# Optimization experiments

Hardware: AMD Instinct MI355X
Metric: run time of the kernel (lower is better)

Reference implementation:

```python
import jax, jax.numpy as jnp
import numpy as np

LN_EPS = 1e-5

def _mha(xq, xkv, in_w, in_b, out_w, out_b, n_heads):
    # torch nn.MultiheadAttention, batch_first=True, dropout=0
    B, S, d = xq.shape
    T = xkv.shape[1]
    dh = d // n_heads
    wq, wk, wv = jnp.split(in_w, 3, axis=0)   # each [d, d]
    bq, bk, bv = jnp.split(in_b, 3)
    q = (xq @ wq.T + bq).reshape(B, S, n_heads, dh).transpose(0, 2, 1, 3)
    k = (xkv @ wk.T + bk).reshape(B, T, n_heads, dh).transpose(0, 2, 1, 3)
    v = (xkv @ wv.T + bv).reshape(B, T, n_heads, dh).transpose(0, 2, 1, 3)
    scores = jnp.einsum('bhsd,bhtd->bhst', q, k) / jnp.sqrt(jnp.asarray(dh, xq.dtype))
    attn = jax.nn.softmax(scores, axis=-1)    # explicit [B,H,S,T] weights (need_weights=True path)
    o = jnp.einsum('bhst,bhtd->bhsd', attn, v)
    o = o.transpose(0, 2, 1, 3).reshape(B, S, d)
    return o @ out_w.T + out_b

def _ln(x, g, b):
    mu = jnp.mean(x, axis=-1, keepdims=True)
    var = jnp.mean(jnp.square(x - mu), axis=-1, keepdims=True)
    return (x - mu) / jnp.sqrt(var + LN_EPS) * g + b

def setup_inputs() -> dict:
    key = jax.random.key(0)
    B, S, T, d, ff = 4, 1024, 1024, 1024, 4096
    ks = jax.random.split(key, 10)
    s = 0.02
    return {
        'x': jax.random.normal(ks[0], (B, S, d), jnp.float32),
        'mem': jax.random.normal(ks[1], (B, T, d), jnp.float32),
        'sa_in_w': jax.random.normal(ks[2], (3 * d, d), jnp.float32) * s,
        'sa_in_b': jnp.zeros((3 * d,), jnp.float32),
        'sa_out_w': jax.random.normal(ks[3], (d, d), jnp.float32) * s,
        'sa_out_b': jnp.zeros((d,), jnp.float32),
        'ca_in_w': jax.random.normal(ks[4], (3 * d, d), jnp.float32) * s,
        'ca_in_b': jnp.zeros((3 * d,), jnp.float32),
        'ca_out_w': jax.random.normal(ks[5], (d, d), jnp.float32) * s,
        'ca_out_b': jnp.zeros((d,), jnp.float32),
        'ff_w1': jax.random.normal(ks[6], (ff, d), jnp.float32) * s,
        'ff_b1': jnp.zeros((ff,), jnp.float32),
        'ff_w2': jax.random.normal(ks[7], (d, ff), jnp.float32) * s,
        'ff_b2': jnp.zeros((d,), jnp.float32),
        'ln1_g': jnp.ones((d,), jnp.float32), 'ln1_b': jnp.zeros((d,), jnp.float32),
        'ln2_g': jnp.ones((d,), jnp.float32), 'ln2_b': jnp.zeros((d,), jnp.float32),
        'ln3_g': jnp.ones((d,), jnp.float32), 'ln3_b': jnp.zeros((d,), jnp.float32),
        'n_heads': 16,
    }

def reference(x, mem, sa_in_w, sa_in_b, sa_out_w, sa_out_b,
              ca_in_w, ca_in_b, ca_out_w, ca_out_b,
              ff_w1, ff_b1, ff_w2, ff_b2,
              ln1_g, ln1_b, ln2_g, ln2_b, ln3_g, ln3_b, n_heads):
    sa = _mha(x, x, sa_in_w, sa_in_b, sa_out_w, sa_out_b, n_heads)
    x = _ln(x + sa, ln1_g, ln1_b)
    ca = _mha(x, mem, ca_in_w, ca_in_b, ca_out_w, ca_out_b, n_heads)
    x = _ln(x + ca, ln2_g, ln2_b)
    h = jax.nn.gelu(x @ ff_w1.T + ff_b1, approximate=False)  # torch nn.GELU default = exact erf
    ff = h @ ff_w2.T + ff_b2
    return _ln(x + ff, ln3_g, ln3_b)
```

## Files before the change

### kernel.cpp

```cpp
#include <hip/hip_runtime.h>
#include <cstddef>

#define D_MODEL 1024
#define SEQ     1024
#define BATCH   4
#define NHEAD   16
#define DH      64
#define FFDIM   4096
#define NTOK    (BATCH*SEQ)

typedef float f32x4  __attribute__((ext_vector_type(4)));
typedef short bf16x8 __attribute__((ext_vector_type(8)));

static __device__ __forceinline__ unsigned short f2bf(float x){
  union { float f; unsigned u; } v; v.f = x;
  unsigned r = v.u + 0x7fffu + ((v.u >> 16) & 1u);
  return (unsigned short)(r >> 16);
}

static __device__ __forceinline__ unsigned short f2bf_t(float x){
  union { float f; unsigned u; } v; v.f = x;
  return (unsigned short)(v.u >> 16);
}

static __device__ __forceinline__ float bf2f(unsigned short h){
  union { unsigned u; float f; } v; v.u = ((unsigned)h) << 16; return v.f;
}

static __device__ __forceinline__ float fast_exp2(float x){
#if __has_builtin(__builtin_amdgcn_exp2f)
  return __builtin_amdgcn_exp2f(x);
#else
  return __expf(x * 0.69314718056f);
#endif
}

static __device__ __forceinline__ void gl_lds16(const void* g, void* l){
  __builtin_amdgcn_global_load_lds((const __attribute__((address_space(1))) void*)g,
                                   (__attribute__((address_space(3))) void*)l, 16, 0, 0);
}

#define WAITV(n) asm volatile("s_waitcnt vmcnt(" #n ")" ::: "memory")
#define WAITL0() asm volatile("s_waitcnt lgkmcnt(0)" ::: "memory")
#define SBAR()   __builtin_amdgcn_s_barrier()
#define SCHED0() __builtin_amdgcn_sched_barrier(0)

static __device__ __forceinline__ int2 swz_tile(int gx, int RX, int RY){
  int id = blockIdx.y * gx + blockIdx.x;
  int x = id & 7, s = id >> 3;
  int nrx = gx / RX;
  int bx = (x % nrx) * RX + (s % RX);
  int by = (x / nrx) * RY + (s / RX);
  return make_int2(bx, by);
}

struct CvtJobs {
  const float* src[8];
  unsigned short* dst[8];
  int n[8];
};

__global__ __launch_bounds__(256) void cvt_kernel(CvtJobs jobs){
  int seg = blockIdx.y;
  const float* s = jobs.src[seg];
  unsigned short* d = jobs.dst[seg];
  int n = jobs.n[seg];
  int stride = gridDim.x * 256 * 4;
  for (int i = (blockIdx.x*256 + threadIdx.x)*4; i < n; i += stride){
    float4 v = *(const float4*)(s + i);
    ushort4 o;
    o.x = f2bf(v.x); o.y = f2bf(v.y); o.z = f2bf(v.z); o.w = f2bf(v.w);
    *(ushort4*)(d + i) = o;
  }
}

static __device__ __forceinline__ int cidx(int row, int col){
  return row*128 + (((col >> 3) ^ (row & 15)) << 3) + (col & 7);
}

template<int EPI>
static __device__ __forceinline__ void gemm_core(
    unsigned short* smem,
    const unsigned short* __restrict__ A,
    const unsigned short* __restrict__ B,
    const float* __restrict__ bias,
    void* __restrict__ out0,
    unsigned short* __restrict__ vt,
    int N, int K, int kbeg, int kend, int row0, int col0,
    int split, int ldout)
{
  unsigned short* As = smem;
  unsigned short* Bs = smem + 128*64;
  const int tid  = threadIdx.x;
  const int w    = tid >> 6, lane = tid & 63;
  const int quad = lane >> 4, l15 = lane & 15;
  const int lr   = lane >> 3, lc = lane & 7;
  const int csrc = lc ^ lr;
  const int sw   = l15 & 7;
  const int wm = (w >> 1) * 64, wn = (w & 1) * 64;

  f32x4 acc[4][4];
  const f32x4 zero4 = {0.f, 0.f, 0.f, 0.f};
  #pragma unroll
  for (int i=0;i<4;i++)
    #pragma unroll
    for (int j=0;j<4;j++)
      acc[i][j] = zero4;

  const unsigned short* Ag = A + (size_t)(row0 + lr)*K + csrc*8;
  const unsigned short* Bg = B + (size_t)(col0 + lr)*K + csrc*8;

  for (int k0 = kbeg; k0 < kend; k0 += 64){
    #pragma unroll
    for (int i=0;i<4;i++){
      gl_lds16(Ag + (size_t)(i*32 + w*8)*K + k0, &As[i*2048 + w*512]);
      gl_lds16(Bg + (size_t)(i*32 + w*8)*K + k0, &Bs[i*2048 + w*512]);
    }
    __syncthreads();
    #pragma unroll
    for (int ks=0; ks<2; ks++){
      bf16x8 af[4], bfr[4];
      #pragma unroll
      for (int i=0;i<4;i++)
        af[i] = *(const bf16x8*)&As[(wm + i*16 + l15)*64 + ((ks*4 + quad) ^ sw)*8];
      #pragma unroll
      for (int j=0;j<4;j++)
        bfr[j] = *(const bf16x8*)&Bs[(wn + j*16 + l15)*64 + ((ks*4 + quad) ^ sw)*8];
      #pragma unroll
      for (int i=0;i<4;i++)
        #pragma unroll
        for (int j=0;j<4;j++)
          acc[i][j] = __builtin_amdgcn_mfma_f32_16x16x32_bf16(af[i], bfr[j], acc[i][j], 0, 0, 0);
    }
    __syncthreads();
  }

  float bj[4];
  #pragma unroll
  for (int j=0;j<4;j++) bj[j] = bias[col0 + wn + j*16 + l15];

  unsigned short* Cs = smem;

  #pragma unroll
  for (int i=0;i<4;i++){
    #pragma unroll
    for (int r=0;r<4;r++){
      int lrow = wm + i*16 + quad*4 + r;
      #pragma unroll
      for (int j=0;j<4;j++){
        int lcol = wn + j*16 + l15;
        float v = acc[i][j][r] + bj[j];
        Cs[cidx(lrow, lcol)] = f2bf(v);
      }
    }
  }
  __syncthreads();

  const int ld = N;
  #pragma unroll
  for (int p=0;p<2;p++){
    int c = p*64 + (tid >> 2);
    unsigned short* dst = (unsigned short*)out0 + (size_t)(row0 + c)*ld + col0;
    #pragma unroll
    for (int k=0;k<4;k++){
      int m = (tid & 3) + k*4;
      bf16x8 val = *(const bf16x8*)&Cs[c*128 + ((m ^ (c & 15)) << 3)];
      *(bf16x8*)(dst + m*8) = val;
    }
  }
}

__global__ __launch_bounds__(256) void gemm_split(
    const unsigned short* A, const unsigned short* B, const float* bias,
    unsigned short* outA, unsigned short* outB, int N, int K)
{
  __shared__ __align__(16) unsigned short smem[2*128*64];
  int2 t = swz_tile(gridDim.x, 4, 8);
  int kseg = K >> 1;
  int kbeg = blockIdx.z * kseg;
  unsigned short* o = blockIdx.z ? outB : outA;
  gemm_core<1>(smem, A, B, bias, o, nullptr, N, K, kbeg, kbeg + kseg,
               t.y*128, t.x*128, 0, 0);
}

#define G256_LDB(bufp) do{                                                    \
    const unsigned short* Bs_ = (bufp) + 16384;                               \
    _Pragma("unroll")                                                         \
    for (int ks=0; ks<2; ks++){                                               \
      const int ch = ((ks*4 + quad) ^ sw)*8;                                  \
      _Pragma("unroll")                                                       \
      for (int j=0;j<4;j++)                                                   \
        bfr[ks][j] = *(const bf16x8*)&Bs_[(wc*64 + j*16 + l15)*64 + ch];      \
    }                                                                         \
  }while(0)

#define G256_LDA(bufp, S) do{                                                 \
    const unsigned short* As_ = (bufp);                                       \
    _Pragma("unroll")                                                         \
    for (int ks=0; ks<2; ks++){                                               \
      const int ch = ((ks*4 + quad) ^ sw)*8;                                  \
      afr[ks][0] = *(const bf16x8*)&As_[(wr*128 + (2*(S)  )*16 + l15)*64 + ch]; \
      afr[ks][1] = *(const bf16x8*)&As_[(wr*128 + (2*(S)+1)*16 + l15)*64 + ch]; \
    }                                                                         \
  }while(0)

#define G256_PH(S) do{                                                        \
    __builtin_amdgcn_s_setprio(1);                                            \
    _Pragma("unroll")                                                         \
    for (int ks=0; ks<2; ks++){                                               \
      _Pragma("unroll")                                                       \
      for (int j=0;j<4;j++){                                                  \
        acc[2*(S)  ][j] = __builtin_amdgcn_mfma_f32_16x16x32_bf16(afr[ks][0], bfr[ks][j], acc[2*(S)  ][j], 0, 0, 0); \
        acc[2*(S)+1][j] = __builtin_amdgcn_mfma_f32_16x16x32_bf16(afr[ks][1], bfr[ks][j], acc[2*(S)+1][j], 0, 0, 0); \
      }                                                                       \
    }                                                                         \
    __builtin_amdgcn_s_setprio(0);                                            \
  }while(0)

#define STG_B4(k0, dstp) do{ unsigned short* _d=(dstp); const int _k=(k0);    \
    gl_lds16(Bg + (size_t)(0*64 + w*8)*K + _k, _d + 16384 + 0*4096 + w*512);  \
    gl_lds16(Bg + (size_t)(1*64 + w*8)*K + _k, _d + 16384 + 1*4096 + w*512);  \
    gl_lds16(Bg + (size_t)(2*64 + w*8)*K + _k, _d + 16384 + 2*4096 + w*512);  \
    gl_lds16(Bg + (size_t)(3*64 + w*8)*K + _k, _d + 16384 + 3*4096 + w*512);  \
  }while(0)
#define STG_A02(k0, dstp) do{ unsigned short* _d=(dstp); const int _k=(k0);   \
    gl_lds16(Ag + (size_t)(0*64 + w*8)*K + _k, _d + 0*4096 + w*512);          \
    gl_lds16(Ag + (size_t)(2*64 + w*8)*K + _k, _d + 2*4096 + w*512);          \
  }while(0)
#define STG_A13(k0, dstp) do{ unsigned short* _d=(dstp); const int _k=(k0);   \
    gl_lds16(Ag + (size_t)(1*64 + w*8)*K + _k, _d + 1*4096 + w*512);          \
    gl_lds16(Ag + (size_t)(3*64 + w*8)*K + _k, _d + 3*4096 + w*512);          \
  }while(0)

template<int EPI>
static __device__ __forceinline__ void gemm256_core(
    unsigned short* smem,
    const unsigned short* __restrict__ A,
    const unsigned short* __restrict__ B,
    const float* __restrict__ bias,
    void* __restrict__ out0,
    unsigned short* __restrict__ vt,
    int N, int K, int kbeg, int kend, int row0, int col0,
    int split, int ldout)
{
  const int tid  = threadIdx.x;
  const int w    = tid >> 6, lane = tid & 63;
  const int quad = lane >> 4, l15 = lane & 15;
  const int lr   = lane >> 3, lc = lane & 7;
  const int csrc = lc ^ lr;
  const int sw   = l15 & 7;
  const int wr   = w >> 2, wc = w & 3;

  f32x4 acc[8][4];
  const f32x4 zero4 = {0.f, 0.f, 0.f, 0.f};
  #pragma unroll
  for (int i=0;i<8;i++)
    #pragma unroll
    for (int j=0;j<4;j++)
      acc[i][j] = zero4;

  bf16x8 bfr[2][4];
  bf16x8 afr[2][2];

  const unsigned short* Ag = A + (size_t)(row0 + lr)*K + csrc*8;
  const unsigned short* Bg = B + (size_t)(col0 + lr)*K + csrc*8;

  unsigned short* buf0 = smem;
  unsigned short* buf1 = smem + 32768;

  STG_B4(kbeg, buf0); STG_A02(kbeg, buf0); STG_A13(kbeg, buf0);
  STG_B4(kbeg + 64, buf1); STG_A02(kbeg + 64, buf1);

  for (int t = 0; t < 16; t++){
    unsigned short* cur = (t & 1) ? buf1 : buf0;
    unsigned short* oth = (t & 1) ? buf0 : buf1;
    const int kb = kbeg + t*64;
    if (t < 15) { WAITV(6); } else { WAITV(0); }
    SBAR(); SCHED0();
    G256_LDB(cur); G256_LDA(cur, 0);
    if (t < 15) STG_A13(kb + 64, oth);
    G256_PH(0);
    WAITL0(); SBAR(); SCHED0();
    G256_LDA(cur, 1);
    if (t < 14) STG_B4(kb + 128, cur);
    G256_PH(1);
    WAITL0(); SBAR(); SCHED0();
    G256_LDA(cur, 2);
    if (t < 14) STG_A02(kb + 128, cur);
    G256_PH(2);
    WAITL0(); SBAR(); SCHED0();
    G256_LDA(cur, 3);
    G256_PH(3);
    WAITL0();
  }
  SBAR(); SCHED0();

  float bj[4];
  #pragma unroll
  for (int j=0;j<4;j++) bj[j] = bias[col0 + wc*64 + j*16 + l15];

  const bool vtile = (EPI == 5) && (col0 >= split);
  unsigned short* Cs = smem;

  #pragma unroll
  for (int i=0;i<8;i++){
    #pragma unroll
    for (int r=0;r<4;r++){
      int lrow = wr*128 + i*16 + quad*4 + r;
      #pragma unroll
      for (int j=0;j<4;j++){
        int lcol = wc*64 + j*16 + l15;
        float v = acc[i][j][r] + bj[j];
        if (EPI == 2){
          float t = 0.7978845608f * (v + 0.044715f * v * v * v);
          float e = __expf(2.f * t);
          float th = 1.f - 2.f * __builtin_amdgcn_rcpf(e + 1.f);
          v = 0.5f * v * (1.f + th);
        }
        int rr = vtile ? lcol : lrow, cc = vtile ? lrow : lcol;
        Cs[rr*256 + (((cc >> 3) ^ (rr & 31)) << 3) + (cc & 7)] = f2bf(v);
      }
    }
  }
  __syncthreads();

  const int ld = (EPI == 5) ? ldout : N;
  #pragma unroll
  for (int p=0;p<2;p++){
    int c = p*128 + (tid >> 2);
    unsigned short* dst;
    if (!vtile){
      dst = (unsigned short*)out0 + (size_t)(row0 + c)*ld + col0;
    } else {
      int colg = (col0 - split) + c;
      int hh = colg >> 6, dd = colg & 63;
      int bb = row0 >> 10, t0 = row0 & 1023;
      dst = vt + ((size_t)(bb*NHEAD + hh)*DH + dd)*SEQ + t0;
    }
    #pragma unroll
    for (int k=0;k<8;k++){
      int m = (tid & 3) + k*4;
      bf16x8 val = *(const bf16x8*)&Cs[c*256 + ((m ^ (c & 31)) << 3)];
      *(bf16x8*)(dst + m*8) = val;
    }
  }
}

__global__ __launch_bounds__(512, 2) void gemm256_ffn1(
    const unsigned short* A, const unsigned short* B, const float* bias,
    unsigned short* out0, int N, int K)
{
  __shared__ __align__(16) unsigned short smem[2*2*256*64];
  int2 t = swz_tile(gridDim.x, 4, 8);
  gemm256_core<2>(smem, A, B, bias, out0, nullptr, N, K, 0, K,
                  t.y*256, t.x*256, 0, 0);
}

__global__ __launch_bounds__(512, 2) void gemm_kv256(
    const unsigned short* xb, const unsigned short* memb,
    const unsigned short* wsa, const unsigned short* wca,
    const float* bsa, const float* bca,
    unsigned short* ksa, unsigned short* vtsa,
    unsigned short* kca, unsigned short* vtca)
{
  __shared__ __align__(16) unsigned short smem[2*2*256*64];
  const int id = blockIdx.x;
  const int xcd = id & 7, s = id >> 3;
  const bool sa = s < 16;
  const int u = sa ? s : s - 16;
  const int bx = (xcd & 3)*2 + (u & 1);
  const int by = (xcd >> 2)*8 + (u >> 1);
  gemm256_core<5>(smem, sa ? xb : memb, sa ? wsa : wca, sa ? bsa : bca,
                  sa ? ksa : kca, sa ? vtsa : vtca,
                  2048, 1024, 0, 1024, by*256, bx*256, 1024, 1024);
}

__global__ __launch_bounds__(512, 2) void gemm256_split4(
    const unsigned short* A, const unsigned short* B, const float* bias,
    unsigned short* o0, unsigned short* o1, unsigned short* o2, unsigned short* o3,
    int N, int K)
{
  __shared__ __align__(16) unsigned short smem[2*2*256*64];
  const int id = blockIdx.x;
  const int xcd = id & 7, s = id >> 3;
  const int z  = xcd >> 1;
  const int bx = s & 3;
  const int by = (xcd & 1)*8 + (s >> 2);
  const int kseg = K >> 2, kbeg = z * kseg;
  unsigned short* o = (z == 0) ? o0 : (z == 1) ? o1 : (z == 2) ? o2 : o3;
  gemm256_core<1>(smem, A, B, bias, o, nullptr, N, K, kbeg, kbeg + kseg,
                  by*256, bx*256, 0, 0);
}

__global__ __launch_bounds__(256) void attn_kernel(
    const unsigned short* __restrict__ Xa,
    const unsigned short* __restrict__ Wq,
    const float* __restrict__ bq,
    const unsigned short* __restrict__ Kp,
    const unsigned short* __restrict__ Vt,
    unsigned short* __restrict__ O)
{
  __shared__ __align__(16) unsigned short Ks[64*64];
  __shared__ __align__(16) unsigned short Vs[64*64];
  __shared__ __align__(16) unsigned short Bu[4*16*72];

  const int tid  = threadIdx.x;
  const int w    = tid >> 6, lane = tid & 63;
  const int quad = lane >> 4, l15 = lane & 15;
  const int lr   = lane >> 3, lc = lane & 7;
  const int csrc = lc ^ lr;
  const int sw   = l15 & 7;
  const int id = blockIdx.x;
  const int xc = id & 7, s = id >> 3;
  const int bh = xc*8 + (s >> 4), qt = s & 15;
  const int b = bh >> 4, h = bh & 15;
  const int q0   = qt * 64;
  const int tok0 = b * SEQ;
  const int hoff = h * DH;

  const f32x4 zero4 = {0.f, 0.f, 0.f, 0.f};

  f32x4 qacc[4];
  #pragma unroll
  for (int dj=0;dj<4;dj++) qacc[dj] = zero4;

  const unsigned short* Ag = Xa + (size_t)(tok0 + q0 + lr)*1024 + csrc*8;
  const unsigned short* Wg = Wq + (size_t)(hoff + lr)*1024 + csrc*8;

  for (int k0 = 0; k0 < 1024; k0 += 64){
    #pragma unroll
    for (int i=0;i<2;i++)
      gl_lds16(Ag + (size_t)(i*32 + w*8)*1024 + k0, &Bu[i*2048 + w*512]);
    #pragma unroll
    for (int i=0;i<2;i++)
      gl_lds16(Wg + (size_t)(i*32 + w*8)*1024 + k0, &Ks[i*2048 + w*512]);
    __syncthreads();
    #pragma unroll
    for (int ks=0; ks<2; ks++){
      const int ch = ((ks*4 + quad) ^ sw)*8;
      bf16x8 af = *(const bf16x8*)&Bu[(w*16 + l15)*64 + ch];
      bf16x8 bfr[4];
      #pragma unroll
      for (int dj=0;dj<4;dj++)
        bfr[dj] = *(const bf16x8*)&Ks[(dj*16 + l15)*64 + ch];
      #pragma unroll
      for (int dj=0;dj<4;dj++)
        qacc[dj] = __builtin_amdgcn_mfma_f32_16x16x32_bf16(af, bfr[dj], qacc[dj], 0, 0, 0);
    }
    __syncthreads();
  }

  {
    const float QSCALE = 0.125f * 1.44269504f;
    float biasv[4];
    #pragma unroll
    for (int dj=0;dj<4;dj++) biasv[dj] = bq[hoff + dj*16 + l15];
    #pragma unroll
    for (int dj=0;dj<4;dj++)
      #pragma unroll
      for (int r=0;r<4;r++){
        int q = w*16 + quad*4 + r;
        int d = dj*16 + l15;
        Bu[q*64 + (((d>>3) ^ (q&7))<<3) + (d&7)] = f2bf((qacc[dj][r] + biasv[dj]) * QSCALE);
      }
  }
  __syncthreads();

  bf16x8 qb[2];
  {
    int row = w*16 + l15;
    qb[0] = *(const bf16x8*)&Bu[row*64 + ((0 + quad) ^ sw)*8];
    qb[1] = *(const bf16x8*)&Bu[row*64 + ((4 + quad) ^ sw)*8];
  }

  float lsum = 0.f;
  f32x4 oacc[4];
  #pragma unroll
  for (int dt=0;dt<4;dt++) oacc[dt] = zero4;

  unsigned short* pw = &Bu[w*16*72];

  for (int kc = 0; kc < SEQ/64; ++kc){
    __syncthreads();
    #pragma unroll
    for (int i=0;i<2;i++){
      int r = i*32 + w*8 + lr;
      gl_lds16(Kp + (size_t)(tok0 + kc*64 + r)*1024 + hoff + csrc*8, &Ks[i*2048 + w*512]);
      gl_lds16(Vt + ((size_t)bh*DH + r)*SEQ + kc*64 + csrc*8,        &Vs[i*2048 + w*512]);
    }
    __syncthreads();

    #pragma unroll
    for (int tj=0;tj<4;tj++){
      bf16x8 ka0 = *(const bf16x8*)&Ks[(tj*16 + l15)*64 + ((0 + quad) ^ sw)*8];
      bf16x8 ka1 = *(const bf16x8*)&Ks[(tj*16 + l15)*64 + ((4 + quad) ^ sw)*8];
      f32x4 z = zero4;
      __builtin_amdgcn_s_setprio(1);
      z = __builtin_amdgcn_mfma_f32_16x16x32_bf16(ka0, qb[0], z, 0, 0, 0);
      z = __builtin_amdgcn_mfma_f32_16x16x32_bf16(ka1, qb[1], z, 0, 0, 0);
      __builtin_amdgcn_s_setprio(0);
      float p0 = fast_exp2(z[0]);
      float p1 = fast_exp2(z[1]);
      float p2 = fast_exp2(z[2]);
      float p3 = fast_exp2(z[3]);
      lsum += (p0 + p1) + (p2 + p3);
      short4 pk;
      pk.x = (short)f2bf_t(p0); pk.y = (short)f2bf_t(p1);
      pk.z = (short)f2bf_t(p2); pk.w = (short)f2bf_t(p3);
      *(short4*)&pw[l15*72 + tj*16 + quad*4] = pk;
    }

    __builtin_amdgcn_s_setprio(1);
    {
      bf16x8 pa0 = *(const bf16x8*)&pw[l15*72 + quad*8];
      bf16x8 pa1 = *(const bf16x8*)&pw[l15*72 + 32 + quad*8];
      #pragma unroll
      for (int dt=0;dt<4;dt++){
        bf16x8 vb0 = *(const bf16x8*)&Vs[(dt*16 + l15)*64 + ((0 + quad) ^ sw)*8];
        bf16x8 vb1 = *(const bf16x8*)&Vs[(dt*16 + l15)*64 + ((4 + quad) ^ sw)*8];
        oacc[dt] = __builtin_amdgcn_mfma_f32_16x16x32_bf16(pa0, vb0, oacc[dt], 0, 0, 0);
        oacc[dt] = __builtin_amdgcn_mfma_f32_16x16x32_bf16(pa1, vb1, oacc[dt], 0, 0, 0);
      }
    }
    __builtin_amdgcn_s_setprio(0);
  }

  lsum += __shfl_xor(lsum, 16);
  lsum += __shfl_xor(lsum, 32);

  __syncthreads();
  unsigned short* OB = Bu;
  #pragma unroll
  for (int r=0;r<4;r++){
    float lv = __shfl(lsum, quad*4 + r);
    float rinv = __builtin_amdgcn_rcpf(lv);
    int q = w*16 + quad*4 + r;
    #pragma unroll
    for (int dt=0;dt<4;dt++){
      int d = dt*16 + l15;
      OB[q*64 + (((d>>3) ^ (q&7))<<3) + (d&7)] = f2bf(oacc[dt][r] * rinv);
    }
  }
  __syncthreads();
  {
    int q = tid >> 2;
    unsigned short* dst = O + (size_t)(tok0 + q0 + q)*D_MODEL + hoff;
    #pragma unroll
    for (int k=0;k<2;k++){
      int m = (tid & 3) + k*4;
      bf16x8 val = *(const bf16x8*)&OB[q*64 + ((m ^ (q & 7)) << 3)];
      *(bf16x8*)(dst + m*8) = val;
    }
  }
}

__global__ __launch_bounds__(256) void ln_kernel(
    const float* __restrict__ resid,
    const unsigned short* __restrict__ d1,
    const unsigned short* __restrict__ d2,
    const unsigned short* __restrict__ d3,
    const unsigned short* __restrict__ d4,
    const float* __restrict__ g, const float* __restrict__ beta,
    float* __restrict__ outf, unsigned short* __restrict__ outb)
{
  const int row = blockIdx.x;
  const int t = threadIdx.x;
  const size_t base = (size_t)row * D_MODEL;
  float4 a = *(const float4*)(resid + base + t*4);
  ushort4 p4 = *(const ushort4*)(d1 + base + t*4);
  ushort4 q4 = *(const ushort4*)(d2 + base + t*4);
  float v0 = a.x + bf2f(p4.x) + bf2f(q4.x);
  float v1 = a.y + bf2f(p4.y) + bf2f(q4.y);
  float v2 = a.z + bf2f(p4.z) + bf2f(q4.z);
  float v3 = a.w + bf2f(p4.w) + bf2f(q4.w);
  if (d3){
    ushort4 r4 = *(const ushort4*)(d3 + base + t*4);
    ushort4 s4 = *(const ushort4*)(d4 + base + t*4);
    v0 += bf2f(r4.x) + bf2f(s4.x);
    v1 += bf2f(r4.y) + bf2f(s4.y);
    v2 += bf2f(r4.z) + bf2f(s4.z);
    v3 += bf2f(r4.w) + bf2f(s4.w);
  }
  float s1 = v0+v1+v2+v3;
  float s2 = v0*v0+v1*v1+v2*v2+v3*v3;
  #pragma unroll
  for (int off=32; off>0; off>>=1){
    s1 += __shfl_down(s1, off);
    s2 += __shfl_down(s2, off);
  }
  __shared__ float red[8];
  const int wid = t >> 6;
  if ((t & 63) == 0){ red[wid*2] = s1; red[wid*2+1] = s2; }
  __syncthreads();
  s1 = red[0]+red[2]+red[4]+red[6];
  s2 = red[1]+red[3]+red[5]+red[7];
  float mean = s1 * (1.f/1024.f);
  float var  = s2 * (1.f/1024.f) - mean*mean;
  float rstd = rsqrtf(var + 1e-5f);
  float4 gg = *(const float4*)(g + t*4);
  float4 bb = *(const float4*)(beta + t*4);
  float y0 = (v0-mean)*rstd*gg.x + bb.x;
  float y1 = (v1-mean)*rstd*gg.y + bb.y;
  float y2 = (v2-mean)*rstd*gg.z + bb.z;
  float y3 = (v3-mean)*rstd*gg.w + bb.w;
  if (outf) *(float4*)(outf + base + t*4) = make_float4(y0,y1,y2,y3);
  if (outb){
    ushort4 o;
    o.x = f2bf(y0); o.y = f2bf(y1); o.z = f2bf(y2); o.w = f2bf(y3);
    *(ushort4*)(outb + base + t*4) = o;
  }
}

extern "C" void kernel_launch(void* const* d_in, const int* in_sizes, int n_in,
                              void* d_out, int out_size, void* d_ws, size_t ws_size,
                              hipStream_t stream)
{
  const float* x        = (const float*)d_in[0];
  const float* mem      = (const float*)d_in[1];
  const float* sa_in_w  = (const float*)d_in[2];
  const float* sa_in_b  = (const float*)d_in[3];
  const float* sa_out_w = (const float*)d_in[4];
  const float* sa_out_b = (const float*)d_in[5];
  const float* ca_in_w  = (const float*)d_in[6];
  const float* ca_in_b  = (const float*)d_in[7];
  const float* ca_out_w = (const float*)d_in[8];
  const float* ca_out_b = (const float*)d_in[9];
  const float* ff_w1    = (const float*)d_in[10];
  const float* ff_b1    = (const float*)d_in[11];
  const float* ff_w2    = (const float*)d_in[12];
  const float* ff_b2    = (const float*)d_in[13];
  const float* ln1_g    = (const float*)d_in[14];
  const float* ln1_b    = (const float*)d_in[15];
  const float* ln2_g    = (const float*)d_in[16];
  const float* ln2_b    = (const float*)d_in[17];
  const float* ln3_g    = (const float*)d_in[18];
  const float* ln3_b    = (const float*)d_in[19];

  char* base = (char*)d_ws;
  size_t off = 0;
  auto alloc = [&](size_t bytes) -> void* {
    void* r = base + off;
    off += (bytes + 255) & ~(size_t)255;
    return r;
  };
  unsigned short* xb     = (unsigned short*)alloc((size_t)NTOK*1024*2);
  unsigned short* memb   = (unsigned short*)alloc((size_t)NTOK*1024*2);
  unsigned short* wsain  = (unsigned short*)alloc((size_t)3072*1024*2);
  unsigned short* wsaout = (unsigned short*)alloc((size_t)1024*1024*2);
  unsigned short* wcain  = (unsigned short*)alloc((size_t)3072*1024*2);
  unsigned short* wcaout = (unsigned short*)alloc((size_t)1024*1024*2);
  unsigned short* wff1   = (unsigned short*)alloc((size_t)4096*1024*2);
  unsigned short* wff2   = (unsigned short*)alloc((size_t)4096*1024*2);
  unsigned short* qkvbuf = (unsigned short*)alloc((size_t)NTOK*3072*2);
  unsigned short* attnb  = (unsigned short*)alloc((size_t)NTOK*1024*2);
  float*          proj   = (float*)alloc((size_t)NTOK*1024*4);
  float*          x1f    = (float*)alloc((size_t)NTOK*1024*4);
  unsigned short* x1b    = (unsigned short*)alloc((size_t)NTOK*1024*2);
  float*          x2f    = (float*)alloc((size_t)NTOK*1024*4);
  unsigned short* x2b    = (unsigned short*)alloc((size_t)NTOK*1024*2);

  unsigned short* ksa  = qkvbuf;
  unsigned short* vtsa = qkvbuf + (size_t)NTOK*1024;
  unsigned short* kca  = qkvbuf + (size_t)NTOK*2048;
  unsigned short* vtca = (unsigned short*)x2f;
  unsigned short* hbuf = qkvbuf;
  unsigned short* pA   = (unsigned short*)proj;
  unsigned short* pB   = (unsigned short*)xb;
  unsigned short* q0p  = (unsigned short*)proj;
  unsigned short* q1p  = (unsigned short*)proj + (size_t)NTOK*1024;
  unsigned short* q2p  = (unsigned short*)x1f;
  unsigned short* q3p  = (unsigned short*)x1f + (size_t)NTOK*1024;

  CvtJobs jobs;
  jobs.src[0]=x;        jobs.dst[0]=xb;     jobs.n[0]=NTOK*1024;
  jobs.src[1]=mem;      jobs.dst[1]=memb;   jobs.n[1]=NTOK*1024;
  jobs.src[2]=sa_in_w;  jobs.dst[2]=wsain;  jobs.n[2]=3072*1024;
  jobs.src[3]=sa_out_w; jobs.dst[3]=wsaout; jobs.n[3]=1024*1024;
  jobs.src[4]=ca_in_w;  jobs.dst[4]=wcain;  jobs.n[4]=3072*1024;
  jobs.src[5]=ca_out_w; jobs.dst[5]=wcaout; jobs.n[5]=1024*1024;
  jobs.src[6]=ff_w1;    jobs.dst[6]=wff1;   jobs.n[6]=4096*1024;
  jobs.src[7]=ff_w2;    jobs.dst[7]=wff2;   jobs.n[7]=4096*1024;
  cvt_kernel<<<dim3(1024,8), 256, 0, stream>>>(jobs);

  gemm_kv256<<<256, 512, 0, stream>>>(xb, memb,
                                      wsain + (size_t)1024*1024, wcain + (size_t)1024*1024,
                                      sa_in_b + 1024, ca_in_b + 1024,
                                      ksa, vtsa, kca, vtca);

  attn_kernel<<<1024, 256, 0, stream>>>(xb, wsain, sa_in_b, ksa, vtsa, attnb);
  gemm_split<<<dim3(8,32,2), 256, 0, stream>>>(attnb, wsaout, sa_out_b, pA, pB, 1024, 1024);
  ln_kernel<<<NTOK, 256, 0, stream>>>(x, pA, pB, nullptr, nullptr, ln1_g, ln1_b, x1f, x1b);

  attn_kernel<<<1024, 256, 0, stream>>>(x1b, wcain, ca_in_b, kca, vtca, attnb);
  gemm_split<<<dim3(8,32,2), 256, 0, stream>>>(attnb, wcaout, ca_out_b, pA, pB, 1024, 1024);
  ln_kernel<<<NTOK, 256, 0, stream>>>(x1f, pA, pB, nullptr, nullptr, ln2_g, ln2_b, x2f, x2b);

  gemm256_ffn1<<<dim3(16,16), 512, 0, stream>>>(x2b, wff1, ff_b1, hbuf, 4096, 1024);
  gemm256_split4<<<256, 512, 0, stream>>>(hbuf, wff2, ff_b2, q0p, q1p, q2p, q3p, 1024, 4096);
  ln_kernel<<<NTOK, 256, 0, stream>>>(x2f, q0p, q1p, q2p, q3p, ln3_g, ln3_b, (float*)d_out, nullptr);
}
```

Measured before the change: 418.6 us.

## Double-buffer LDS staging in 128x128 GEMM core with phased prefetch

The 128x128 GEMM core moves from single-buffer load-sync-compute to a two-buffer software pipeline. Global-to-LDS loads for the next one or two K tiles are split into chunks and issued between the MFMA phases of the current tile, with vmcnt waits, barriers and raised wave priority around the MFMAs. The goal is to hide global load latency behind matrix math. In exchange, LDS per block doubles, which may lower occupancy, and more barriers are added per K step.

```diff
diff --git a/kernel.cpp b/kernel.cpp
--- a/kernel.cpp
+++ b/kernel.cpp
@@ -78,6 +78,52 @@
   return row*128 + (((col >> 3) ^ (row & 15)) << 3) + (col & 7);
 }
 
+#define STG128_B4(k0, dstp) do{ unsigned short* _d=(dstp); const int _k=(k0); \
+    gl_lds16(Bg + (size_t)(0*32 + w*8)*K + _k, _d + 8192 + 0*2048 + w*512);   \
+    gl_lds16(Bg + (size_t)(1*32 + w*8)*K + _k, _d + 8192 + 1*2048 + w*512);   \
+    gl_lds16(Bg + (size_t)(2*32 + w*8)*K + _k, _d + 8192 + 2*2048 + w*512);   \
+    gl_lds16(Bg + (size_t)(3*32 + w*8)*K + _k, _d + 8192 + 3*2048 + w*512);   \
+  }while(0)
+#define STG128_A02(k0, dstp) do{ unsigned short* _d=(dstp); const int _k=(k0);\
+    gl_lds16(Ag + (size_t)(0*32 + w*8)*K + _k, _d + 0*2048 + w*512);          \
+    gl_lds16(Ag + (size_t)(2*32 + w*8)*K + _k, _d + 2*2048 + w*512);          \
+  }while(0)
+#define STG128_A13(k0, dstp) do{ unsigned short* _d=(dstp); const int _k=(k0);\
+    gl_lds16(Ag + (size_t)(1*32 + w*8)*K + _k, _d + 1*2048 + w*512);          \
+    gl_lds16(Ag + (size_t)(3*32 + w*8)*K + _k, _d + 3*2048 + w*512);          \
+  }while(0)
+
+#define G128_LDB(bufp) do{                                                    \
+    const unsigned short* Bs_ = (bufp) + 8192;                                \
+    _Pragma("unroll")                                                         \
+    for (int ks=0; ks<2; ks++){                                               \
+      const int ch = ((ks*4 + quad) ^ sw)*8;                                  \
+      _Pragma("unroll")                                                       \
+      for (int j=0;j<4;j++)                                                   \
+        bfr[ks][j] = *(const bf16x8*)&Bs_[(wn + j*16 + l15)*64 + ch];         \
+    }                                                                         \
+  }while(0)
+
+#define G128_LDA(bufp, S) do{                                                 \
+    const unsigned short* As_ = (bufp);                                       \
+    _Pragma("unroll")                                                         \
+    for (int ks=0; ks<2; ks++){                                               \
+      const int ch = ((ks*4 + quad) ^ sw)*8;                                  \
+      afr[ks] = *(const bf16x8*)&As_[(wm + (S)*16 + l15)*64 + ch];            \
+    }                                                                         \
+  }while(0)
+
+#define G128_PH(S) do{                                                        \
+    __builtin_amdgcn_s_setprio(1);                                            \
+    _Pragma("unroll")                                                         \
+    for (int ks=0; ks<2; ks++){                                               \
+      _Pragma("unroll")                                                       \
+      for (int j=0;j<4;j++)                                                   \
+        acc[S][j] = __builtin_amdgcn_mfma_f32_16x16x32_bf16(afr[ks], bfr[ks][j], acc[S][j], 0, 0, 0); \
+    }                                                                         \
+    __builtin_amdgcn_s_setprio(0);                                            \
+  }while(0)
+
 template<int EPI>
 static __device__ __forceinline__ void gemm_core(
     unsigned short* smem,
@@ -89,8 +135,6 @@
     int N, int K, int kbeg, int kend, int row0, int col0,
     int split, int ldout)
 {
-  unsigned short* As = smem;
-  unsigned short* Bs = smem + 128*64;
   const int tid  = threadIdx.x;
   const int w    = tid >> 6, lane = tid & 63;
   const int quad = lane >> 4, l15 = lane & 15;
@@ -107,33 +151,42 @@
     for (int j=0;j<4;j++)
       acc[i][j] = zero4;
 
+  bf16x8 bfr[2][4];
+  bf16x8 afr[2];
+
   const unsigned short* Ag = A + (size_t)(row0 + lr)*K + csrc*8;
   const unsigned short* Bg = B + (size_t)(col0 + lr)*K + csrc*8;
 
-  for (int k0 = kbeg; k0 < kend; k0 += 64){
-    #pragma unroll
-    for (int i=0;i<4;i++){
-      gl_lds16(Ag + (size_t)(i*32 + w*8)*K + k0, &As[i*2048 + w*512]);
-      gl_lds16(Bg + (size_t)(i*32 + w*8)*K + k0, &Bs[i*2048 + w*512]);
-    }
-    __syncthreads();
-    #pragma unroll
-    for (int ks=0; ks<2; ks++){
-      bf16x8 af[4], bfr[4];
-      #pragma unroll
-      for (int i=0;i<4;i++)
-        af[i] = *(const bf16x8*)&As[(wm + i*16 + l15)*64 + ((ks*4 + quad) ^ sw)*8];
-      #pragma unroll
-      for (int j=0;j<4;j++)
-        bfr[j] = *(const bf16x8*)&Bs[(wn + j*16 + l15)*64 + ((ks*4 + quad) ^ sw)*8];
-      #pragma unroll
-      for (int i=0;i<4;i++)
-        #pragma unroll
-        for (int j=0;j<4;j++)
-          acc[i][j] = __builtin_amdgcn_mfma_f32_16x16x32_bf16(af[i], bfr[j], acc[i][j], 0, 0, 0);
-    }
-    __syncthreads();
-  }
+  unsigned short* buf0 = smem;
+  unsigned short* buf1 = smem + 16384;
+
+  const int NT = (kend - kbeg) >> 6;
+  STG128_B4(kbeg, buf0); STG128_A02(kbeg, buf0); STG128_A13(kbeg, buf0);
+  STG128_B4(kbeg + 64, buf1); STG128_A02(kbeg + 64, buf1);
+
+  for (int t = 0; t < NT; t++){
+    unsigned short* cur = (t & 1) ? buf1 : buf0;
+    unsigned short* oth = (t & 1) ? buf0 : buf1;
+    const int kb = kbeg + t*64;
+    if (t < NT-1) { WAITV(6); } else { WAITV(0); }
+    SBAR(); SCHED0();
+    G128_LDB(cur); G128_LDA(cur, 0);
+    if (t+1 < NT) STG128_A13(kb + 64, oth);
+    G128_PH(0);
+    WAITL0(); SBAR(); SCHED0();
+    G128_LDA(cur, 1);
+    if (t+2 < NT) STG128_B4(kb + 128, cur);
+    G128_PH(1);
+    WAITL0(); SBAR(); SCHED0();
+    G128_LDA(cur, 2);
+    if (t+2 < NT) STG128_A02(kb + 128, cur);
+    G128_PH(2);
+    WAITL0(); SBAR(); SCHED0();
+    G128_LDA(cur, 3);
+    G128_PH(3);
+    WAITL0();
+  }
+  SBAR(); SCHED0();
 
   float bj[4];
   #pragma unroll
@@ -174,7 +227,7 @@
     const unsigned short* A, const unsigned short* B, const float* bias,
     unsigned short* outA, unsigned short* outB, int N, int K)
 {
-  __shared__ __align__(16) unsigned short smem[2*128*64];
+  __shared__ __align__(16) unsigned short smem[2*2*128*64];
   int2 t = swz_tile(gridDim.x, 4, 8);
   int kseg = K >> 1;
   int kbeg = blockIdx.z * kseg;
```

Result: no change. 422.9 us (+1.0%).
